# Optimization experiments

Measured on AMD Instinct MI355X. Metric: run time of the kernel, lower is better.

The kernel has to match this reference:

```python
import jax, jax.numpy as jnp
import numpy as np

B, T, D, H = 2, 2048, 1024, 16
DH = D // H

def setup_inputs() -> dict:
    key = jax.random.key(0)
    k1, k2, k3 = jax.random.split(key, 3)
    x = jax.random.normal(k1, (B, T, D), dtype=jnp.float32)
    Wqkv = jax.random.normal(k2, (D, 3 * D), dtype=jnp.float32) * (1.0 / np.sqrt(D))
    Wo = jax.random.normal(k3, (D, D), dtype=jnp.float32) * (1.0 / np.sqrt(D))
    return {"x": x, "Wqkv": Wqkv, "Wo": Wo}

def reference(x, Wqkv, Wo):
    b, t, d = x.shape
    qkv = x @ Wqkv                      # [B,T,3D]
    q, k, v = jnp.split(qkv, 3, axis=-1)
    q = q.reshape(b, t, H, DH)          # [B,T,H,DH]
    k = k.reshape(b, t, H, DH)
    v = v.reshape(b, t, H, DH)
    scale = 1.0 / np.sqrt(DH).astype(np.float32)
    scores = jnp.einsum('bqhd,bkhd->bhqk', q, k) * scale  # [B,H,T,T]
    causal = jnp.tril(jnp.ones((t, t), dtype=bool))       # True = keep
    scores = jnp.where(causal, scores, jnp.finfo(scores.dtype).min)
    attn = jax.nn.softmax(scores, axis=-1)
    y = jnp.einsum('bhqk,bkhd->bqhd', attn, v)            # [B,T,H,DH]
    y = y.reshape(b, t, d)
    return y @ Wo
```

## Files before the change

kernel.cpp:

```cpp
#include <hip/hip_runtime.h>
#include <stdint.h>

typedef __attribute__((ext_vector_type(8))) short short8;
typedef __attribute__((ext_vector_type(8))) __bf16 bf16x8;
typedef __attribute__((ext_vector_type(4))) float f32x4;
typedef __attribute__((ext_vector_type(2))) unsigned int u32x2;

#define T_SEQ 2048

static __device__ __forceinline__ ushort f2bf(float f) {
  uint32_t u = __float_as_uint(f);
  u += 0x7fffu + ((u >> 16) & 1u);
  return (ushort)(u >> 16);
}

static __device__ __forceinline__ uint32_t cvtpk(float lo, float hi) {
  uint32_t r;
  asm("v_cvt_pk_bf16_f32 %0, %1, %2" : "=v"(r) : "v"(lo), "v"(hi));
  return r;
}

static __device__ __forceinline__ f32x4 mfma16(short8 a, short8 b, f32x4 c) {
  return __builtin_amdgcn_mfma_f32_16x16x32_bf16(
      __builtin_bit_cast(bf16x8, a), __builtin_bit_cast(bf16x8, b), c, 0, 0, 0);
}

static __device__ __forceinline__ void gload16(const ushort* g, char* l) {
  __builtin_amdgcn_global_load_lds(
      (const __attribute__((address_space(1))) void*)g,
      (__attribute__((address_space(3))) void*)l, 16, 0, 0);
}

__global__ __launch_bounds__(256) void cvt_bf16_k(const float* __restrict__ in,
                                                  ushort* __restrict__ out) {
  int i = (blockIdx.x * 256 + threadIdx.x) * 8;
  float4 a = *(const float4*)(in + i);
  float4 b = *(const float4*)(in + i + 4);
  short8 o;
  ((ushort*)&o)[0] = f2bf(a.x); ((ushort*)&o)[1] = f2bf(a.y);
  ((ushort*)&o)[2] = f2bf(a.z); ((ushort*)&o)[3] = f2bf(a.w);
  ((ushort*)&o)[4] = f2bf(b.x); ((ushort*)&o)[5] = f2bf(b.y);
  ((ushort*)&o)[6] = f2bf(b.z); ((ushort*)&o)[7] = f2bf(b.w);
  *(short8*)(out + i) = o;
}

__global__ __launch_bounds__(256) void transpose_cvt2_k(
    const float* __restrict__ Wqkv, const float* __restrict__ Wo,
    ushort* __restrict__ WqkvT, ushort* __restrict__ WoT) {
  __shared__ ushort t[64][65];
  const int K = 1024;
  const float* in;
  ushort* out;
  int N, byl;
  if (blockIdx.y < 48) { in = Wqkv; out = WqkvT; N = 3072; byl = blockIdx.y; }
  else                 { in = Wo;   out = WoT;   N = 1024; byl = blockIdx.y - 48; }
  const int bk = blockIdx.x * 64, bn = byl * 64;
  const int r = threadIdx.x >> 2, c0 = (threadIdx.x & 3) << 4;
  const float* src = in + (size_t)(bk + r) * N + bn + c0;
#pragma unroll
  for (int q = 0; q < 4; ++q) {
    float4 a = *(const float4*)(src + q * 4);
    t[r][c0 + q * 4 + 0] = f2bf(a.x);
    t[r][c0 + q * 4 + 1] = f2bf(a.y);
    t[r][c0 + q * 4 + 2] = f2bf(a.z);
    t[r][c0 + q * 4 + 3] = f2bf(a.w);
  }
  __syncthreads();
  short8 o0, o1;
#pragma unroll
  for (int j = 0; j < 8; ++j) {
    ((ushort*)&o0)[j] = t[c0 + j][r];
    ((ushort*)&o1)[j] = t[c0 + 8 + j][r];
  }
  ushort* dst = out + (size_t)(bn + r) * K + bk + c0;
  *(short8*)(dst) = o0;
  *(short8*)(dst + 8) = o1;
}

__global__ __launch_bounds__(256) void gemm_bt(const ushort* __restrict__ A,
                                               const ushort* __restrict__ Bt,
                                               void* __restrict__ Cv,
                                               int Mdim, int Ndim, int Kdim,
                                               int f32out) {
  __shared__ char sA[128 * 128];
  __shared__ char sB[128 * 128];
  const int tid = threadIdx.x;
  const int lane = tid & 63, wid = tid >> 6;
  const int wm = wid >> 1, wn = wid & 1;
  const int lc = lane & 15, lg = lane >> 4;
  const int bm = blockIdx.x * 128, bn = blockIdx.y * 128;
  const int lane16 = lane << 4;

  f32x4 acc[4][4] = {};

  for (int k0 = 0; k0 < Kdim; k0 += 64) {
    __syncthreads();
#pragma unroll
    for (int i = 0; i < 4; ++i) {
      int v = tid + i * 256;
      int row = v >> 3;
      int cbl = (v & 7) << 4;
      int ce = (cbl ^ ((row & 7) << 4)) >> 1;
      char* la = sA + ((v << 4) - lane16);
      char* lb = sB + ((v << 4) - lane16);
      gload16(A + (size_t)(bm + row) * Kdim + k0 + ce, la);
      gload16(Bt + (size_t)(bn + row) * Kdim + k0 + ce, lb);
    }
    __syncthreads();
#pragma unroll
    for (int ks = 0; ks < 2; ++ks) {
      const int kb = ks * 64 + lg * 16;
      short8 af[4], bfr[4];
#pragma unroll
      for (int m = 0; m < 4; ++m) {
        int row = wm * 64 + m * 16 + lc;
        af[m] = *(const short8*)&sA[(row << 7) + (kb ^ ((row & 7) << 4))];
      }
#pragma unroll
      for (int n = 0; n < 4; ++n) {
        int row = wn * 64 + n * 16 + lc;
        bfr[n] = *(const short8*)&sB[(row << 7) + (kb ^ ((row & 7) << 4))];
      }
#pragma unroll
      for (int m = 0; m < 4; ++m)
#pragma unroll
        for (int n = 0; n < 4; ++n)
          acc[m][n] = mfma16(af[m], bfr[n], acc[m][n]);
    }
  }
#pragma unroll
  for (int m = 0; m < 4; ++m) {
    int rowb = bm + wm * 64 + m * 16 + lg * 4;
#pragma unroll
    for (int n = 0; n < 4; ++n) {
      int col = bn + wn * 64 + n * 16 + lc;
      if (f32out) {
        float* C = (float*)Cv;
#pragma unroll
        for (int r = 0; r < 4; ++r)
          C[(size_t)(rowb + r) * Ndim + col] = acc[m][n][r];
      } else {
        ushort* C = (ushort*)Cv;
#pragma unroll
        for (int r = 0; r < 4; ++r)
          C[(size_t)(rowb + r) * Ndim + col] = f2bf(acc[m][n][r]);
      }
    }
  }
}

__global__ __launch_bounds__(512) void attn_k(const ushort* __restrict__ qkv,
                                              ushort* __restrict__ Y) {
  __shared__ char sK[8192];
  __shared__ char sV[8192];
  __shared__ char sP[16384];
  __shared__ float sL[8][16];
  const int tid = threadIdx.x;
  const int lane = tid & 63, wid = tid >> 6;
  const int lc = lane & 15, lg = lane >> 4;
  const int orig = blockIdx.x;
  const int xcd = orig & 7, slot = orig >> 3;
  int tile, bhl;
  if (slot < 32) { tile = slot >> 2;              bhl = slot & 3; }
  else           { tile = 15 - ((slot - 32) >> 2); bhl = (slot - 32) & 3; }
  const int bh = xcd * 4 + bhl;
  const int b = bh >> 4, h = bh & 15;
  char* sPw = sP + (wid << 11);

  const ushort* base = qkv + (size_t)b * T_SEQ * 3072 + h * 64;
  const int q0 = tile * 128 + wid * 16;

  const int kt = tid >> 3, kce = (tid & 7) << 3, kcb = kce << 1;
  const int ksw = (kt & 7) << 4;
  const int vt = tid & 63, vd0 = (tid >> 6) << 3;
  const ushort* kbase = base + 1024;
  const ushort* vbase = base + 2048;

  short8 qf[2];
#pragma unroll
  for (int ks = 0; ks < 2; ++ks)
    qf[ks] = *(const short8*)(base + (size_t)(q0 + lc) * 3072 + ks * 32 + lg * 8);

  f32x4 o[4] = {};
  float lsum = 0.f;

  const float cexp = 0.125f * 1.4426950408889634f;
  const int nkb = 2 * (tile + 1);
  const int qmaxw = q0 + 15;

  short8 kr = *(const short8*)(kbase + (size_t)kt * 3072 + kce);
  short8 vr = *(const short8*)(vbase + (size_t)vt * 3072 + vd0);

  for (int kb = 0; kb < nkb; ++kb) {
    __syncthreads();
    *(short8*)&sK[(kt << 7) + (kcb ^ ksw)] = kr;
#pragma unroll
    for (int j = 0; j < 8; ++j) {
      int d = vd0 + j;
      *(ushort*)&sV[(d << 7) + ((2 * vt) ^ ((d & 7) << 4))] = ((const ushort*)&vr)[j];
    }
    __syncthreads();
    if (kb + 1 < nkb) {
      kr = *(const short8*)(kbase + (size_t)((kb + 1) * 64 + kt) * 3072 + kce);
      vr = *(const short8*)(vbase + (size_t)((kb + 1) * 64 + vt) * 3072 + vd0);
    }
    if (kb * 64 > qmaxw) continue;

    f32x4 S[4] = {};
    __builtin_amdgcn_s_setprio(1);
#pragma unroll
    for (int ks = 0; ks < 2; ++ks) {
      int kbyt = ks * 64 + lg * 16;
      short8 kf[4];
#pragma unroll
      for (int n = 0; n < 4; ++n) {
        int row = n * 16 + lc;
        kf[n] = *(const short8*)&sK[(row << 7) + (kbyt ^ ((row & 7) << 4))];
      }
#pragma unroll
      for (int n = 0; n < 4; ++n)
        S[n] = mfma16(kf[n], qf[ks], S[n]);
    }
    __builtin_amdgcn_s_setprio(0);

    const bool diag = (kb * 64 + 63 > q0);
    {
      int q = q0 + lc;
      float lacc = 0.f;
#pragma unroll
      for (int n = 0; n < 4; ++n) {
        int kg = kb * 64 + n * 16 + lg * 4;
        f32x4 pe;
#pragma unroll
        for (int r = 0; r < 4; ++r) {
          pe[r] = exp2f(S[n][r] * cexp);
          if (diag && (kg + r > q)) pe[r] = 0.f;
        }
        lacc += (pe[0] + pe[1]) + (pe[2] + pe[3]);
        u32x2 w;
        w[0] = cvtpk(pe[0], pe[1]);
        w[1] = cvtpk(pe[2], pe[3]);
        int colb = n * 32 + lg * 8;
        *(u32x2*)&sPw[(lc << 7) + (colb ^ ((lc & 7) << 4))] = w;
      }
      lsum += lacc;
    }
    asm volatile("" ::: "memory");
    __builtin_amdgcn_s_setprio(1);
#pragma unroll
    for (int ks = 0; ks < 2; ++ks) {
      int kbyt = ks * 64 + lg * 16;
      short8 pf = *(const short8*)&sPw[(lc << 7) + (kbyt ^ ((lc & 7) << 4))];
      short8 vf[4];
#pragma unroll
      for (int dn = 0; dn < 4; ++dn) {
        int row = dn * 16 + lc;
        vf[dn] = *(const short8*)&sV[(row << 7) + (kbyt ^ ((row & 7) << 4))];
      }
#pragma unroll
      for (int dn = 0; dn < 4; ++dn)
        o[dn] = mfma16(pf, vf[dn], o[dn]);
    }
    __builtin_amdgcn_s_setprio(0);
  }
  {
    float v = lsum;
    v += __shfl_xor(v, 16);
    v += __shfl_xor(v, 32);
    sL[wid][lc] = 1.0f / v;
  }
  asm volatile("" ::: "memory");
  {
    float lr[4];
#pragma unroll
    for (int r = 0; r < 4; ++r) lr[r] = sL[wid][lg * 4 + r];
#pragma unroll
    for (int dn = 0; dn < 4; ++dn) {
#pragma unroll
      for (int r = 0; r < 4; ++r) {
        int t = q0 + lg * 4 + r;
        Y[(size_t)(b * T_SEQ + t) * 1024 + h * 64 + dn * 16 + lc] =
            f2bf(o[dn][r] * lr[r]);
      }
    }
  }
}

extern "C" void kernel_launch(void* const* d_in, const int* in_sizes, int n_in,
                              void* d_out, int out_size, void* d_ws, size_t ws_size,
                              hipStream_t stream) {
  const float* x    = (const float*)d_in[0];
  const float* Wqkv = (const float*)d_in[1];
  const float* Wo   = (const float*)d_in[2];
  for (int i = 0; i < n_in; ++i) {
    if (in_sizes[i] == 4194304) x = (const float*)d_in[i];
    else if (in_sizes[i] == 3145728) Wqkv = (const float*)d_in[i];
    else if (in_sizes[i] == 1048576) Wo = (const float*)d_in[i];
  }
  float* out = (float*)d_out;

  ushort* xb    = (ushort*)d_ws;
  ushort* WqkvT = xb + (size_t)4096 * 1024;
  ushort* WoT   = WqkvT + (size_t)3072 * 1024;
  ushort* QKV   = WoT + (size_t)1024 * 1024;
  ushort* Yb    = QKV + (size_t)4096 * 3072;

  cvt_bf16_k<<<2048, 256, 0, stream>>>(x, xb);
  transpose_cvt2_k<<<dim3(16, 64), 256, 0, stream>>>(Wqkv, Wo, WqkvT, WoT);
  gemm_bt<<<dim3(32, 24), 256, 0, stream>>>(xb, WqkvT, QKV, 4096, 3072, 1024, 0);
  attn_k<<<512, 512, 0, stream>>>(QKV, Yb);
  gemm_bt<<<dim3(32, 8), 256, 0, stream>>>(Yb, WoT, out, 4096, 1024, 1024, 1);
}
```

Before: 125.7 us.

## Split causal attention KV range across blocks with atomic fp32 accumulation

Attention work is redistributed into 24 balanced chunks per head group: the heavier query tiles have their key range split in two, so 768 blocks of similar cost replace 512 uneven ones. Partial unnormalized outputs and row sums go to fp32 buffers via atomicAdd. A memset and a new normalize kernel then divide by the sums and convert to bf16. This targets the load imbalance of causal attention, at the cost of extra memset, atomic traffic, an additional kernel launch and an fp32 round trip. It relies on a fixed max-free exp (no running max), as the original did.

```diff
diff --git a/kernel.cpp b/kernel.cpp
--- a/kernel.cpp
+++ b/kernel.cpp
@@ -149,20 +149,27 @@
   }
 }
 
+static __device__ const signed char CH_TILE[24] =
+    {15,15,14,13,12,11,10, 9, 8, 7,14, 6,13, 5,12, 4,11, 3,10, 2, 9, 1, 8, 0};
+static __device__ const signed char CH_KB0[24] =
+    { 0,16, 0, 0, 0, 0, 0, 0, 0, 0,16, 0,16, 0,16, 0,16, 0,16, 0,16, 0,16, 0};
+static __device__ const signed char CH_KB1[24] =
+    {16,32,16,16,16,16,16,16,16,16,30,14,28,12,26,10,24, 8,22, 6,20, 4,18, 2};
+
 __global__ __launch_bounds__(512) void attn_k(const ushort* __restrict__ qkv,
-                                              ushort* __restrict__ Y) {
+                                              float* __restrict__ Yacc,
+                                              float* __restrict__ lsumg) {
   __shared__ char sK[8192];
   __shared__ char sV[8192];
   __shared__ char sP[16384];
-  __shared__ float sL[8][16];
   const int tid = threadIdx.x;
   const int lane = tid & 63, wid = tid >> 6;
   const int lc = lane & 15, lg = lane >> 4;
   const int orig = blockIdx.x;
-  const int xcd = orig & 7, slot = orig >> 3;
-  int tile, bhl;
-  if (slot < 32) { tile = slot >> 2;              bhl = slot & 3; }
-  else           { tile = 15 - ((slot - 32) >> 2); bhl = (slot - 32) & 3; }
+  const int xcd = orig & 7, s = orig >> 3;
+  const int c = s >> 2, bhl = s & 3;
+  const int tile = CH_TILE[c];
+  const int kb0 = CH_KB0[c], kb1 = CH_KB1[c];
   const int bh = xcd * 4 + bhl;
   const int b = bh >> 4, h = bh & 15;
   char* sPw = sP + (wid << 11);
@@ -185,13 +192,12 @@
   float lsum = 0.f;
 
   const float cexp = 0.125f * 1.4426950408889634f;
-  const int nkb = 2 * (tile + 1);
   const int qmaxw = q0 + 15;
 
-  short8 kr = *(const short8*)(kbase + (size_t)kt * 3072 + kce);
-  short8 vr = *(const short8*)(vbase + (size_t)vt * 3072 + vd0);
-
-  for (int kb = 0; kb < nkb; ++kb) {
+  short8 kr = *(const short8*)(kbase + (size_t)(kb0 * 64 + kt) * 3072 + kce);
+  short8 vr = *(const short8*)(vbase + (size_t)(kb0 * 64 + vt) * 3072 + vd0);
+
+  for (int kb = kb0; kb < kb1; ++kb) {
     __syncthreads();
     *(short8*)&sK[(kt << 7) + (kcb ^ ksw)] = kr;
 #pragma unroll
@@ -200,7 +206,7 @@
       *(ushort*)&sV[(d << 7) + ((2 * vt) ^ ((d & 7) << 4))] = ((const ushort*)&vr)[j];
     }
     __syncthreads();
-    if (kb + 1 < nkb) {
+    if (kb + 1 < kb1) {
       kr = *(const short8*)(kbase + (size_t)((kb + 1) * 64 + kt) * 3072 + kce);
       vr = *(const short8*)(vbase + (size_t)((kb + 1) * 64 + vt) * 3072 + vd0);
     }
@@ -267,23 +273,36 @@
     float v = lsum;
     v += __shfl_xor(v, 16);
     v += __shfl_xor(v, 32);
-    sL[wid][lc] = 1.0f / v;
-  }
-  asm volatile("" ::: "memory");
-  {
-    float lr[4];
-#pragma unroll
-    for (int r = 0; r < 4; ++r) lr[r] = sL[wid][lg * 4 + r];
-#pragma unroll
-    for (int dn = 0; dn < 4; ++dn) {
-#pragma unroll
-      for (int r = 0; r < 4; ++r) {
-        int t = q0 + lg * 4 + r;
-        Y[(size_t)(b * T_SEQ + t) * 1024 + h * 64 + dn * 16 + lc] =
-            f2bf(o[dn][r] * lr[r]);
-      }
-    }
-  }
+    if (lg == 0) atomicAdd(&lsumg[(size_t)bh * T_SEQ + q0 + lc], v);
+  }
+#pragma unroll
+  for (int dn = 0; dn < 4; ++dn) {
+#pragma unroll
+    for (int r = 0; r < 4; ++r) {
+      int t = q0 + lg * 4 + r;
+      atomicAdd(&Yacc[(size_t)(b * T_SEQ + t) * 1024 + h * 64 + dn * 16 + lc],
+                o[dn][r]);
+    }
+  }
+}
+
+__global__ __launch_bounds__(256) void normalize_k(const float* __restrict__ Yacc,
+                                                   const float* __restrict__ lsumg,
+                                                   ushort* __restrict__ Ybf) {
+  int i = (blockIdx.x * 256 + threadIdx.x) * 8;
+  int row = i >> 10;
+  int col = i & 1023;
+  int b = row >> 11, tq = row & 2047;
+  int h = col >> 6;
+  float inv = 1.0f / lsumg[(size_t)((b << 4) + h) * T_SEQ + tq];
+  float4 a = *(const float4*)(Yacc + i);
+  float4 c = *(const float4*)(Yacc + i + 4);
+  short8 o;
+  ((ushort*)&o)[0] = f2bf(a.x * inv); ((ushort*)&o)[1] = f2bf(a.y * inv);
+  ((ushort*)&o)[2] = f2bf(a.z * inv); ((ushort*)&o)[3] = f2bf(a.w * inv);
+  ((ushort*)&o)[4] = f2bf(c.x * inv); ((ushort*)&o)[5] = f2bf(c.y * inv);
+  ((ushort*)&o)[6] = f2bf(c.z * inv); ((ushort*)&o)[7] = f2bf(c.w * inv);
+  *(short8*)(Ybf + i) = o;
 }
 
 extern "C" void kernel_launch(void* const* d_in, const int* in_sizes, int n_in,
@@ -299,15 +318,20 @@
   }
   float* out = (float*)d_out;
 
-  ushort* xb    = (ushort*)d_ws;
-  ushort* WqkvT = xb + (size_t)4096 * 1024;
-  ushort* WoT   = WqkvT + (size_t)3072 * 1024;
-  ushort* QKV   = WoT + (size_t)1024 * 1024;
-  ushort* Yb    = QKV + (size_t)4096 * 3072;
+  char* w = (char*)d_ws;
+  ushort* xb    = (ushort*)w;
+  ushort* WqkvT = (ushort*)(w + 8388608);
+  float*  Yacc  = (float*)w;
+  float*  lsumg = (float*)(w + 16777216);
+  ushort* WoT   = (ushort*)(w + 17039360);
+  ushort* QKV   = (ushort*)(w + 19136512);
+  ushort* Ybf   = (ushort*)(w + 44302336);
 
   cvt_bf16_k<<<2048, 256, 0, stream>>>(x, xb);
   transpose_cvt2_k<<<dim3(16, 64), 256, 0, stream>>>(Wqkv, Wo, WqkvT, WoT);
   gemm_bt<<<dim3(32, 24), 256, 0, stream>>>(xb, WqkvT, QKV, 4096, 3072, 1024, 0);
-  attn_k<<<512, 512, 0, stream>>>(QKV, Yb);
-  gemm_bt<<<dim3(32, 8), 256, 0, stream>>>(Yb, WoT, out, 4096, 1024, 1024, 1);
-}
+  hipMemsetAsync(Yacc, 0, 16777216 + 262144, stream);
+  attn_k<<<768, 512, 0, stream>>>(QKV, Yacc, lsumg);
+  normalize_k<<<2048, 256, 0, stream>>>(Yacc, lsumg, Ybf);
+  gemm_bt<<<dim3(32, 8), 256, 0, stream>>>(Ybf, WoT, out, 4096, 1024, 1024, 1);
+}
```

Result: slower. 142.2 us (+13.1%).

## Use 256x256 double-buffered GEMM kernel for the QKV projection

Applied to the files above, without the earlier changes.

Adds a new 512-thread GEMM kernel with 256x256 output tiles and a K step of 64. It double-buffers LDS stages with async global loads and uses setprio around the MFMA bursts. The QKV projection now uses it in place of the 128x128 gemm_bt. The larger tiles raise operand reuse and the double buffering overlaps loads with compute. In exchange the grid drops to 192 blocks, fewer than the CU count, and LDS use per block grows to 128KB.

```diff
diff --git a/kernel.cpp b/kernel.cpp
--- a/kernel.cpp
+++ b/kernel.cpp
@@ -75,6 +75,91 @@
   ushort* dst = out + (size_t)(bn + r) * K + bk + c0;
   *(short8*)(dst) = o0;
   *(short8*)(dst + 8) = o1;
+}
+
+__global__ __launch_bounds__(512) void gemm256(const ushort* __restrict__ A,
+                                               const ushort* __restrict__ Bt,
+                                               ushort* __restrict__ C,
+                                               int Ndim) {
+  __shared__ char sA[2][32768];
+  __shared__ char sB[2][32768];
+  const int tid = threadIdx.x;
+  const int lane = tid & 63, wid = tid >> 6;
+  const int wm = wid >> 2, wn = wid & 3;
+  const int lc = lane & 15, lg = lane >> 4;
+  const int bm = blockIdx.x * 256, bn = blockIdx.y * 256;
+  const int lane16 = lane << 4;
+
+  f32x4 acc[8][4] = {};
+
+#define STAGE256(tt, bb)                                                   \
+  do {                                                                     \
+    _Pragma("unroll") for (int i_ = 0; i_ < 4; ++i_) {                     \
+      int v_ = tid + i_ * 512;                                             \
+      int row_ = v_ >> 3;                                                  \
+      int cbl_ = (v_ & 7) << 4;                                            \
+      int ce_ = (cbl_ ^ ((row_ & 7) << 4)) >> 1;                           \
+      char* la_ = sA[bb] + ((v_ << 4) - lane16);                           \
+      char* lb_ = sB[bb] + ((v_ << 4) - lane16);                           \
+      gload16(A + (size_t)(bm + row_) * 1024 + (tt) * 64 + ce_, la_);      \
+      gload16(Bt + (size_t)(bn + row_) * 1024 + (tt) * 64 + ce_, lb_);     \
+    }                                                                      \
+  } while (0)
+
+  STAGE256(0, 0);
+  STAGE256(1, 1);
+
+  for (int t = 0; t < 16; ++t) {
+    const int cur = t & 1;
+    if (t < 15) asm volatile("s_waitcnt vmcnt(8)" ::: "memory");
+    else        asm volatile("s_waitcnt vmcnt(0)" ::: "memory");
+    __builtin_amdgcn_s_barrier();
+    __builtin_amdgcn_sched_barrier(0);
+#pragma unroll
+    for (int ks = 0; ks < 2; ++ks) {
+      const int kb = ks * 64 + lg * 16;
+      short8 bf[4];
+#pragma unroll
+      for (int nf = 0; nf < 4; ++nf) {
+        int row = wn * 64 + nf * 16 + lc;
+        bf[nf] = *(const short8*)&sB[cur][(row << 7) + (kb ^ ((row & 7) << 4))];
+      }
+#pragma unroll
+      for (int mh = 0; mh < 2; ++mh) {
+        short8 af[4];
+#pragma unroll
+        for (int mf = 0; mf < 4; ++mf) {
+          int row = wm * 128 + mh * 64 + mf * 16 + lc;
+          af[mf] = *(const short8*)&sA[cur][(row << 7) + (kb ^ ((row & 7) << 4))];
+        }
+        __builtin_amdgcn_s_setprio(1);
+#pragma unroll
+        for (int mf = 0; mf < 4; ++mf)
+#pragma unroll
+          for (int nf = 0; nf < 4; ++nf)
+            acc[mh * 4 + mf][nf] = mfma16(af[mf], bf[nf], acc[mh * 4 + mf][nf]);
+        __builtin_amdgcn_s_setprio(0);
+      }
+    }
+    asm volatile("s_waitcnt lgkmcnt(0)" ::: "memory");
+    __builtin_amdgcn_sched_barrier(0);
+    __builtin_amdgcn_s_barrier();
+    __builtin_amdgcn_sched_barrier(0);
+    if (t + 2 < 16) STAGE256(t + 2, cur);
+  }
+#undef STAGE256
+
+#pragma unroll
+  for (int mf = 0; mf < 8; ++mf) {
+    int rowb = bm + wm * 128 + mf * 16 + lg * 4;
+#pragma unroll
+    for (int nf = 0; nf < 4; ++nf) {
+      int col = bn + wn * 64 + nf * 16 + lc;
+#pragma unroll
+      for (int r = 0; r < 4; ++r)
+        C[(size_t)(rowb + r) * Ndim + col] = f2bf(acc[mf][nf][r]);
+    }
+  }
 }
 
 __global__ __launch_bounds__(256) void gemm_bt(const ushort* __restrict__ A,
@@ -307,7 +392,7 @@
 
   cvt_bf16_k<<<2048, 256, 0, stream>>>(x, xb);
   transpose_cvt2_k<<<dim3(16, 64), 256, 0, stream>>>(Wqkv, Wo, WqkvT, WoT);
-  gemm_bt<<<dim3(32, 24), 256, 0, stream>>>(xb, WqkvT, QKV, 4096, 3072, 1024, 0);
+  gemm256<<<dim3(16, 12), 512, 0, stream>>>(xb, WqkvT, QKV, 3072);
   attn_k<<<512, 512, 0, stream>>>(QKV, Yb);
   gemm_bt<<<dim3(32, 8), 256, 0, stream>>>(Yb, WoT, out, 4096, 1024, 1024, 1);
 }
```

Result: faster. 120.1 us (-4.4%).
